# Kernel tuning notes

Measured on AMD Instinct MI355X. Metric: run time of the kernel, lower is better.

Reference implementation:

```python
import jax, jax.numpy as jnp
import numpy as np

EMBED_DIM = 1024
EXPAND_RATIO = 128  # head_dim; n_heads = EMBED_DIM // EXPAND_RATIO = 8
B, N = 4, 2048


def setup_inputs() -> dict:
    key = jax.random.key(0)
    ks = jax.random.split(key, 6)
    std = 0.02
    d = EMBED_DIM
    return {
        "x": jax.random.normal(ks[0], (B, N, d), dtype=jnp.float32),
        "Wq": jax.random.normal(ks[1], (d, d), dtype=jnp.float32) * std,
        "Wk": jax.random.normal(ks[2], (d, d), dtype=jnp.float32) * std,
        "Wv": jax.random.normal(ks[3], (d, d), dtype=jnp.float32) * std,
        "Wo": jax.random.normal(ks[4], (d, d), dtype=jnp.float32) * std,
        "norm_w": jnp.ones((d,), dtype=jnp.float32),
    }


def _rmsnorm(x, w, eps=1e-6):
    return x * jax.lax.rsqrt(jnp.mean(x * x, axis=-1, keepdims=True) + eps) * w


def _gla_scan(q, k, v, g):
    # q,k,v,g: [b, n, h, d]; state S: [b, h, d_k, d_v]
    b, n, h, d = q.shape
    qs, ks_, vs, gs = (jnp.moveaxis(t, 1, 0) for t in (q, k, v, g))  # [n,b,h,d]
    S0 = jnp.zeros((b, h, d, d), dtype=q.dtype)

    def step(S, inp):
        q_t, k_t, v_t, g_t = inp
        # S_t = diag(exp(g_t)) S_{t-1} + k_t^T v_t (gate on key dim)
        S = jnp.exp(g_t)[..., :, None] * S + k_t[..., :, None] * v_t[..., None, :]
        o_t = jnp.einsum('bhk,bhkv->bhv', q_t, S)
        return S, o_t

    _, outs = jax.lax.scan(step, S0, (qs, ks_, vs, gs))
    return jnp.moveaxis(outs, 0, 1)  # [b, n, h, d]


def reference(x, Wq, Wk, Wv, Wo, norm_w):
    b, n, D = x.shape
    hd = EXPAND_RATIO
    h = D // hd

    q = jax.nn.silu(x @ Wq.T)          # q_activation = silu
    f = jax.nn.sigmoid(x @ Wk.T)       # f = sigmoid(k_proj(x))
    log_f = jax.nn.log_sigmoid(f)      # faithful: logsigmoid applied to f (lower_bound=None path)
    k = 1.0 - f
    v = x @ Wv.T

    def split_heads(t):
        return t.reshape(b, n, h, hd)

    out = _gla_scan(split_heads(q), split_heads(k), split_heads(v), split_heads(log_f))
    out = out.reshape(b, n, D)
    out = _rmsnorm(out, norm_w)        # norm_pos='ogate', no output gate
    return out @ Wo.T
```

## Files before the change

kernel.cpp:

```cpp
#include <hip/hip_runtime.h>
#include <cstdint>
#include <cstddef>


typedef unsigned short u16;
using f32x4  = __attribute__((ext_vector_type(4))) float;
using bf16x8 = __attribute__((ext_vector_type(8))) short;

__device__ __forceinline__ float bf2f(u16 u) {
  union { unsigned int i; float f; } v; v.i = ((unsigned int)u) << 16; return v.f;
}
__device__ __forceinline__ u16 f2bf(float f) {
  union { float f; unsigned int i; } v; v.f = f;
  unsigned int r = v.i + 0x7fffu + ((v.i >> 16) & 1u);
  return (u16)(r >> 16);
}
__device__ __forceinline__ void async_load16(const void* g, void* l) {
  __builtin_amdgcn_global_load_lds(
      (const __attribute__((address_space(1))) unsigned int*)(uintptr_t)g,
      (__attribute__((address_space(3))) unsigned int*)(uintptr_t)l, 16, 0, 0);
}
__device__ __forceinline__ float logsig01(float f) {
  float u = f * f;
  return -0.69314718f + 0.5f * f + u * (-0.125f + u * (0.0052083335f - u * 3.472222e-4f));
}

__device__ __forceinline__ void gemm128_core(const u16* __restrict__ Ag, const u16* __restrict__ Bg,
                                             u16* smem, f32x4 (&acc)[4][4]) {
  const int tid = threadIdx.x;
  const int lane = tid & 63, wave = tid >> 6;
  const int wm = (wave & 1) * 64, wn = (wave >> 1) * 64;
  const int r = lane & 15, quad = lane >> 4;
  const int xk = (r >> 1) & 3;
  const u16* baseA = smem + (wm + r) * 32 + ((quad ^ xk) & 3) * 8;
  const u16* baseB = smem + 4096 + (wn + r) * 32 + ((quad ^ xk) & 3) * 8;
  const int soff = (tid >> 2) * 1024 + (((tid & 3) ^ ((tid >> 3) & 3)) * 8);
  u16* dA = smem + wave * 512;
  u16* dB = smem + 4096 + wave * 512;
#pragma unroll
  for (int it = 0; it < 2; ++it) {
    async_load16(Ag + it * 65536 + soff, dA + it * 2048);
    async_load16(Bg + it * 65536 + soff, dB + it * 2048);
  }
#pragma unroll 2
  for (int kt = 0; kt < 32; ++kt) {
    const int cb = (kt & 1) * 8192;
    __syncthreads();
    if (kt < 31) {
      const int nb = ((kt + 1) & 1) * 8192;
      const u16* As = Ag + (kt + 1) * 32 + soff;
      const u16* Bs = Bg + (kt + 1) * 32 + soff;
#pragma unroll
      for (int it = 0; it < 2; ++it) {
        async_load16(As + it * 65536, dA + nb + it * 2048);
        async_load16(Bs + it * 65536, dB + nb + it * 2048);
      }
    }
    bf16x8 af[4], bv[4];
#pragma unroll
    for (int i = 0; i < 4; ++i) af[i] = *(const bf16x8*)(baseA + cb + i * 512);
#pragma unroll
    for (int j = 0; j < 4; ++j) bv[j] = *(const bf16x8*)(baseB + cb + j * 512);
#pragma unroll
    for (int i = 0; i < 4; ++i)
#pragma unroll
      for (int j = 0; j < 4; ++j)
        acc[i][j] = __builtin_amdgcn_mfma_f32_16x16x32_bf16(af[i], bv[j], acc[i][j], 0, 0, 0);
  }
}

__device__ __forceinline__ void gemm64_core(const u16* __restrict__ Ag, const u16* __restrict__ Bg,
                                            u16* smem, f32x4 (&acc)[2][4]) {
  const int tid = threadIdx.x;
  const int lane = tid & 63, wave = tid >> 6;
  const int wm = (wave & 1) * 32, wn = (wave >> 1) * 64;
  const int r = lane & 15, quad = lane >> 4;
  const int xk = (r >> 1) & 3;
  const u16* baseA = smem + (wm + r) * 32 + ((quad ^ xk) & 3) * 8;
  const u16* baseB = smem + 2048 + (wn + r) * 32 + ((quad ^ xk) & 3) * 8;
  const int soff = (tid >> 2) * 1024 + (((tid & 3) ^ ((tid >> 3) & 3)) * 8);
  u16* dA = smem + wave * 512;
  u16* dB = smem + 2048 + wave * 512;
  async_load16(Ag + soff, dA);
  async_load16(Bg + soff, dB);
  async_load16(Bg + 65536 + soff, dB + 2048);
#pragma unroll 2
  for (int kt = 0; kt < 32; ++kt) {
    const int cb = (kt & 1) * 6144;
    __syncthreads();
    if (kt < 31) {
      const int nb = ((kt + 1) & 1) * 6144;
      const u16* As = Ag + (kt + 1) * 32 + soff;
      const u16* Bs = Bg + (kt + 1) * 32 + soff;
      async_load16(As, dA + nb);
      async_load16(Bs, dB + nb);
      async_load16(Bs + 65536, dB + nb + 2048);
    }
    bf16x8 af[2], bv[4];
#pragma unroll
    for (int i = 0; i < 2; ++i) af[i] = *(const bf16x8*)(baseA + cb + i * 512);
#pragma unroll
    for (int j = 0; j < 4; ++j) bv[j] = *(const bf16x8*)(baseB + cb + j * 512);
#pragma unroll
    for (int i = 0; i < 2; ++i)
#pragma unroll
      for (int j = 0; j < 4; ++j)
        acc[i][j] = __builtin_amdgcn_mfma_f32_16x16x32_bf16(af[i], bv[j], acc[i][j], 0, 0, 0);
  }
}

__global__ __launch_bounds__(256) void cast_all(
    const float* __restrict__ x, const float* __restrict__ w0, const float* __restrict__ w1,
    const float* __restrict__ w2, const float* __restrict__ w3, const float* __restrict__ nw,
    u16* __restrict__ xd, u16* __restrict__ d0, u16* __restrict__ d1,
    u16* __restrict__ d2, u16* __restrict__ d3, float* __restrict__ Sv) {
  const int blk = blockIdx.x;
  if (blk >= 12288) {
    Sv[(blk - 12288) * 256 + threadIdx.x] = 0.f;
    return;
  }
  const float* src;
  u16* dst;
  int i;
  bool fold = false;
  if (blk < 8192) {
    src = x; dst = xd; i = blk * 256 + threadIdx.x;
  } else {
    int wb = blk - 8192, which = wb >> 10;
    i = (wb & 1023) * 256 + threadIdx.x;
    src = which == 0 ? w0 : (which == 1 ? w1 : (which == 2 ? w2 : w3));
    dst = which == 0 ? d0 : (which == 1 ? d1 : (which == 2 ? d2 : d3));
    fold = (which == 3);
  }
  float4 v = ((const float4*)src)[i];
  if (fold) {
    float4 wv = ((const float4*)nw)[i & 255];
    v.x *= wv.x; v.y *= wv.y; v.z *= wv.z; v.w *= wv.w;
  }
  unsigned int lo = (unsigned)f2bf(v.x) | ((unsigned)f2bf(v.y) << 16);
  unsigned int hi = (unsigned)f2bf(v.z) | ((unsigned)f2bf(v.w) << 16);
  ((uint2*)dst)[i] = make_uint2(lo, hi);
}

__global__ __launch_bounds__(256) void hgru_gemm_qkv(
    const u16* __restrict__ Xb, const u16* __restrict__ Wqb, const u16* __restrict__ Wkb,
    const u16* __restrict__ Wvb, u16* __restrict__ Qb, u16* __restrict__ Kb,
    u16* __restrict__ Vb) {
  __shared__ alignas(16) u16 smem[12288];
  const int which = blockIdx.y >> 3, bn = blockIdx.y & 7;
  const u16* W = which == 0 ? Wqb : (which == 1 ? Wkb : Wvb);
  const u16* Ag = Xb + (size_t)blockIdx.x * 64 * 1024;
  const u16* Bg = W + (size_t)bn * 128 * 1024;
  f32x4 acc[2][4] = {};
  gemm64_core(Ag, Bg, smem, acc);
  const int tid = threadIdx.x, lane = tid & 63, wave = tid >> 6;
  const int wm = (wave & 1) * 32, wn = (wave >> 1) * 64;
  const int r = lane & 15, quad = lane >> 4;

  __syncthreads();
#pragma unroll
  for (int i = 0; i < 2; ++i)
#pragma unroll
    for (int j = 0; j < 4; ++j)
#pragma unroll
      for (int reg = 0; reg < 4; ++reg) {
        int ml = wm + i * 16 + quad * 4 + reg;
        int nl = wn + j * 16 + r;
        float z = acc[i][j][reg];
        float v;
        if (which == 0)      v = z / (1.f + __expf(-z));
        else if (which == 1) { float ek = __expf(-z); v = ek / (1.f + ek); }
        else                 v = z;
        smem[ml * 136 + nl] = f2bf(v);
      }
  __syncthreads();

  u16* __restrict__ dst = which == 0 ? Qb : (which == 1 ? Kb : Vb);
  const int row16 = tid >> 4, seg = tid & 15;
#pragma unroll
  for (int p = 0; p < 4; ++p) {
    int row = row16 + p * 16;
    *(uint4*)(dst + (size_t)(blockIdx.x * 64 + row) * 1024 + bn * 128 + seg * 8) =
        *(const uint4*)(smem + row * 136 + seg * 8);
  }
}

__global__ __launch_bounds__(256, 4) void hgru_scan(
    const u16* __restrict__ Qg, const u16* __restrict__ Kg, const u16* __restrict__ Vg,
    u16* __restrict__ O, float* __restrict__ Ssum) {
  __shared__ alignas(16) char smem[40448];
  u16* sKt  = (u16*)(smem);
  u16* sVt1 = (u16*)(smem + 10240);
  u16* sK   = (u16*)(smem + 15360);
  u16* sQ   = (u16*)(smem + 24064);
  u16* sVt2 = (u16*)(smem + 32768);
  u16* sAm  = (u16*)(smem + 37888);
  u16* sU   = (u16*)(smem);
  u16* sO   = (u16*)(smem + 17408);

  const int tid = threadIdx.x, blk = blockIdx.x;
  const int vh = blk & 1, c = (blk >> 1) & 63, bh = blk >> 7, h = bh & 7, bb_ = bh >> 3;
  const size_t rb = (size_t)(bb_ * 2048 + c * 32) * 1024 + h * 128;
  const bool haveP = (c > 0);
  const size_t rb1 = haveP ? rb - 32 * 1024 : rb;

  const int lane = tid & 63, wave = tid >> 6;
  const int r = lane & 15, quad = lane >> 4;
  const int ts = tid & 31, g8 = tid >> 5;

  uint4 V2 = *(const uint4*)(Vg + rb  + (size_t)ts * 1024 + vh * 64 + g8 * 8);
  uint4 V1 = *(const uint4*)(Vg + rb1 + (size_t)ts * 1024 + vh * 64 + g8 * 8);
  { const u16* vp = (const u16*)&V2;
#pragma unroll
    for (int e = 0; e < 8; ++e) sVt2[(g8 * 8 + e) * 40 + ts] = vp[e]; }
  if (haveP) {
    const u16* vp = (const u16*)&V1;
#pragma unroll
    for (int e = 0; e < 8; ++e) sVt1[(g8 * 8 + e) * 40 + ts] = vp[e];
  }

  const int col = tid & 127;
  if (tid < 128) {
    if (haveP) {
      const u16* kc = Kg + rb1 + col;
      unsigned int kraw[16];
      float bC = 0.f;
#pragma unroll
      for (int t = 0; t < 16; ++t) {
        unsigned int a = kc[(size_t)(2 * t) * 1024];
        unsigned int b = kc[(size_t)(2 * t + 1) * 1024];
        kraw[t] = a | (b << 16);
        bC += logsig01(1.f - bf2f((u16)a)) + logsig01(1.f - bf2f((u16)b));
      }
      float run = 0.f;
#pragma unroll
      for (int t = 0; t < 16; ++t) {
        float ka = bf2f((u16)(kraw[t] & 0xffff));
        float kb = bf2f((u16)(kraw[t] >> 16));
        run += logsig01(1.f - ka);
        sKt[col * 40 + 2 * t]     = f2bf(ka * __expf(bC - run));
        run += logsig01(1.f - kb);
        sKt[col * 40 + 2 * t + 1] = f2bf(kb * __expf(bC - run));
      }
    }
  } else {
    const u16* kc = Kg + rb + col;
    const u16* qc = Qg + rb + col;
    float run = 0.f;
#pragma unroll
    for (int t = 0; t < 32; ++t) {
      u16 ku = kc[(size_t)t * 1024];
      u16 qu = qc[(size_t)t * 1024];
      float kv = bf2f(ku);
      run += logsig01(1.f - kv);
      sQ[t * 136 + col] = f2bf(bf2f(qu) * __expf(run));
      sK[t * 136 + col] = f2bf(kv * __expf(-run));
    }
  }
  __syncthreads();

  f32x4 accU[2][4] = {};
  const int vm = (wave & 1) * 32, in = (wave >> 1) * 64;
  if (haveP) {
#pragma unroll
    for (int mi = 0; mi < 2; ++mi) {
      bf16x8 af = *(const bf16x8*)(sVt1 + (vm + mi * 16 + r) * 40 + quad * 8);
#pragma unroll
      for (int nj = 0; nj < 4; ++nj) {
        bf16x8 bv = *(const bf16x8*)(sKt + (in + nj * 16 + r) * 40 + quad * 8);
        accU[mi][nj] = __builtin_amdgcn_mfma_f32_16x16x32_bf16(af, bv, accU[mi][nj], 0, 0, 0);
      }
    }
  }
  { const int mi = wave & 1, nj = wave >> 1;
    f32x4 a1 = {0.f, 0.f, 0.f, 0.f};
#pragma unroll
    for (int ks = 0; ks < 4; ++ks) {
      bf16x8 af = *(const bf16x8*)(sQ + (mi * 16 + r) * 136 + ks * 32 + quad * 8);
      bf16x8 bk = *(const bf16x8*)(sK + (nj * 16 + r) * 136 + ks * 32 + quad * 8);
      a1 = __builtin_amdgcn_mfma_f32_16x16x32_bf16(af, bk, a1, 0, 0, 0);
    }
#pragma unroll
    for (int reg = 0; reg < 4; ++reg) {
      int t = mi * 16 + quad * 4 + reg, s = nj * 16 + r;
      sAm[t * 40 + s] = (s <= t) ? f2bf(a1[reg]) : (u16)0;
    } }
  __syncthreads();

  if (haveP) {
#pragma unroll
    for (int mi = 0; mi < 2; ++mi)
#pragma unroll
      for (int nj = 0; nj < 4; ++nj)
#pragma unroll
        for (int reg = 0; reg < 4; ++reg) {
          int vl = vm + mi * 16 + quad * 4 + reg;
          int i  = in + nj * 16 + r;
          sU[vl * 136 + i] = f2bf(accU[mi][nj][reg]);
        }
  }
  __syncthreads();

  { const int mi = wave & 1, no = (wave >> 1) * 32;
    bf16x8 af0 = *(const bf16x8*)(sAm + (mi * 16 + r) * 40 + quad * 8);
    bf16x8 afq[4];
    if (haveP) {
#pragma unroll
      for (int ks = 0; ks < 4; ++ks)
        afq[ks] = *(const bf16x8*)(sQ + (mi * 16 + r) * 136 + ks * 32 + quad * 8);
    }
    f32x4 ssq = {0.f, 0.f, 0.f, 0.f};
#pragma unroll
    for (int j = 0; j < 2; ++j) {
      f32x4 acc2 = {0.f, 0.f, 0.f, 0.f};
      bf16x8 bv0 = *(const bf16x8*)(sVt2 + (no + j * 16 + r) * 40 + quad * 8);
      acc2 = __builtin_amdgcn_mfma_f32_16x16x32_bf16(af0, bv0, acc2, 0, 0, 0);
      if (haveP) {
#pragma unroll
        for (int ks = 0; ks < 4; ++ks) {
          bf16x8 bs = *(const bf16x8*)(sU + (no + j * 16 + r) * 136 + ks * 32 + quad * 8);
          acc2 = __builtin_amdgcn_mfma_f32_16x16x32_bf16(afq[ks], bs, acc2, 0, 0, 0);
        }
      }
      ssq += acc2 * acc2;
#pragma unroll
      for (int reg = 0; reg < 4; ++reg) {
        int t = mi * 16 + quad * 4 + reg;
        sO[t * 72 + no + j * 16 + r] = f2bf(acc2[reg]);
      }
    }
    const int rowg = bb_ * 2048 + c * 32 + mi * 16 + quad * 4;
#pragma unroll
    for (int reg = 0; reg < 4; ++reg) {
      float v = ssq[reg];
      v += __shfl_xor(v, 1); v += __shfl_xor(v, 2);
      v += __shfl_xor(v, 4); v += __shfl_xor(v, 8);
      if (r == 0) atomicAdd(&Ssum[rowg + reg], v);
    } }
  __syncthreads();

  { const int row = tid >> 3, seg = tid & 7;
    *(uint4*)(O + rb + (size_t)row * 1024 + vh * 64 + seg * 8) =
        *(const uint4*)(sO + row * 72 + seg * 8); }
}

__global__ __launch_bounds__(256) void hgru_gemm_out(const u16* __restrict__ Ab,
                                                     const u16* __restrict__ Wob,
                                                     const float* __restrict__ Ssum,
                                                     float* __restrict__ out) {
  __shared__ alignas(16) u16 smem[16384];
  const u16* Ag = Ab + (size_t)blockIdx.x * 128 * 1024;
  const u16* Bg = Wob + (size_t)blockIdx.y * 128 * 1024;
  f32x4 acc[4][4] = {};
  gemm128_core(Ag, Bg, smem, acc);
  const int tid = threadIdx.x, lane = tid & 63, wave = tid >> 6;
  const int wm = (wave & 1) * 64, wn = (wave >> 1) * 64;
  const int r = lane & 15, quad = lane >> 4;
#pragma unroll
  for (int i = 0; i < 4; ++i)
#pragma unroll
    for (int reg = 0; reg < 4; ++reg) {
      int m = blockIdx.x * 128 + wm + i * 16 + quad * 4 + reg;
      float sm = rsqrtf(Ssum[m] * (1.f / 1024.f) + 1e-6f);
#pragma unroll
      for (int j = 0; j < 4; ++j) {
        int n = blockIdx.y * 128 + wn + j * 16 + r;
        out[(size_t)m * 1024 + n] = acc[i][j][reg] * sm;
      }
    }
}

extern "C" void kernel_launch(void* const* d_in, const int* in_sizes, int n_in,
                              void* d_out, int out_size, void* d_ws, size_t ws_size,
                              hipStream_t stream) {
  const float* x  = (const float*)d_in[0];
  const float* Wq = (const float*)d_in[1];
  const float* Wk = (const float*)d_in[2];
  const float* Wv = (const float*)d_in[3];
  const float* Wo = (const float*)d_in[4];
  const float* nw = (const float*)d_in[5];
  float* out = (float*)d_out;
  char* ws = (char*)d_ws;

  u16* Xb   = (u16*)(ws + 0);
  u16* Wqb  = (u16*)(ws + 16777216);
  u16* Wkb  = (u16*)(ws + 18874368);
  u16* Wvb  = (u16*)(ws + 20971520);
  u16* Wob  = (u16*)(ws + 23068672);
  u16* Qb   = (u16*)(ws + 25165824);
  u16* Kb   = (u16*)(ws + 41943040);
  u16* Vb   = (u16*)(ws + 58720256);
  u16* Obf  = (u16*)(ws + 75497472);
  float* Sv = (float*)(ws + 92274688);

  cast_all<<<12320, 256, 0, stream>>>(x, Wq, Wk, Wv, Wo, nw, Xb, Wqb, Wkb, Wvb, Wob, Sv);

  dim3 gq(128, 24);
  hgru_gemm_qkv<<<gq, 256, 0, stream>>>(Xb, Wqb, Wkb, Wvb, Qb, Kb, Vb);
  hgru_scan<<<4096, 256, 0, stream>>>(Qb, Kb, Vb, Obf, Sv);
  dim3 go(64, 8);
  hgru_gemm_out<<<go, 256, 0, stream>>>(Obf, Wob, Sv, out);
}
```

Measured before the change: 245.8 us.

## Enlarge QKV GEMM tile to 256x128 with 512-thread blocks

The QKV projection GEMM moves from 64x128 tiles on 256 threads to 256x128 tiles on 512 threads. Each wave now computes a 64x64 sub-tile with 4x4 MFMA accumulators. This raises arithmetic intensity and reuses each weight tile across four times more rows, cutting global/LDS traffic per FLOP. The epilogue is split into two phases so it can reuse the staging buffer. The trade-off is a grid of only 768 blocks for 256 CUs, more registers per thread, and double the LDS.

New measurement: 617.8 us. +151.4%, slower.

```diff
diff --git a/kernel.cpp b/kernel.cpp
--- a/kernel.cpp
+++ b/kernel.cpp
@@ -69,46 +69,6 @@
   }
 }
 
-__device__ __forceinline__ void gemm64_core(const u16* __restrict__ Ag, const u16* __restrict__ Bg,
-                                            u16* smem, f32x4 (&acc)[2][4]) {
-  const int tid = threadIdx.x;
-  const int lane = tid & 63, wave = tid >> 6;
-  const int wm = (wave & 1) * 32, wn = (wave >> 1) * 64;
-  const int r = lane & 15, quad = lane >> 4;
-  const int xk = (r >> 1) & 3;
-  const u16* baseA = smem + (wm + r) * 32 + ((quad ^ xk) & 3) * 8;
-  const u16* baseB = smem + 2048 + (wn + r) * 32 + ((quad ^ xk) & 3) * 8;
-  const int soff = (tid >> 2) * 1024 + (((tid & 3) ^ ((tid >> 3) & 3)) * 8);
-  u16* dA = smem + wave * 512;
-  u16* dB = smem + 2048 + wave * 512;
-  async_load16(Ag + soff, dA);
-  async_load16(Bg + soff, dB);
-  async_load16(Bg + 65536 + soff, dB + 2048);
-#pragma unroll 2
-  for (int kt = 0; kt < 32; ++kt) {
-    const int cb = (kt & 1) * 6144;
-    __syncthreads();
-    if (kt < 31) {
-      const int nb = ((kt + 1) & 1) * 6144;
-      const u16* As = Ag + (kt + 1) * 32 + soff;
-      const u16* Bs = Bg + (kt + 1) * 32 + soff;
-      async_load16(As, dA + nb);
-      async_load16(Bs, dB + nb);
-      async_load16(Bs + 65536, dB + nb + 2048);
-    }
-    bf16x8 af[2], bv[4];
-#pragma unroll
-    for (int i = 0; i < 2; ++i) af[i] = *(const bf16x8*)(baseA + cb + i * 512);
-#pragma unroll
-    for (int j = 0; j < 4; ++j) bv[j] = *(const bf16x8*)(baseB + cb + j * 512);
-#pragma unroll
-    for (int i = 0; i < 2; ++i)
-#pragma unroll
-      for (int j = 0; j < 4; ++j)
-        acc[i][j] = __builtin_amdgcn_mfma_f32_16x16x32_bf16(af[i], bv[j], acc[i][j], 0, 0, 0);
-  }
-}
-
 __global__ __launch_bounds__(256) void cast_all(
     const float* __restrict__ x, const float* __restrict__ w0, const float* __restrict__ w1,
     const float* __restrict__ w2, const float* __restrict__ w3, const float* __restrict__ nw,
@@ -142,46 +102,87 @@
   ((uint2*)dst)[i] = make_uint2(lo, hi);
 }
 
-__global__ __launch_bounds__(256) void hgru_gemm_qkv(
+__global__ __launch_bounds__(512, 6) void hgru_gemm_qkv(
     const u16* __restrict__ Xb, const u16* __restrict__ Wqb, const u16* __restrict__ Wkb,
     const u16* __restrict__ Wvb, u16* __restrict__ Qb, u16* __restrict__ Kb,
     u16* __restrict__ Vb) {
-  __shared__ alignas(16) u16 smem[12288];
+  __shared__ alignas(16) u16 smem[24576];
   const int which = blockIdx.y >> 3, bn = blockIdx.y & 7;
   const u16* W = which == 0 ? Wqb : (which == 1 ? Wkb : Wvb);
-  const u16* Ag = Xb + (size_t)blockIdx.x * 64 * 1024;
+  const u16* Ag = Xb + (size_t)blockIdx.x * 256 * 1024;
   const u16* Bg = W + (size_t)bn * 128 * 1024;
-  f32x4 acc[2][4] = {};
-  gemm64_core(Ag, Bg, smem, acc);
-  const int tid = threadIdx.x, lane = tid & 63, wave = tid >> 6;
-  const int wm = (wave & 1) * 32, wn = (wave >> 1) * 64;
+
+  const int tid = threadIdx.x;
+  const int lane = tid & 63, wave = tid >> 6;
+  const int wr = wave >> 1, wc = wave & 1;
   const int r = lane & 15, quad = lane >> 4;
-
-  __syncthreads();
-#pragma unroll
-  for (int i = 0; i < 2; ++i)
-#pragma unroll
-    for (int j = 0; j < 4; ++j)
-#pragma unroll
-      for (int reg = 0; reg < 4; ++reg) {
-        int ml = wm + i * 16 + quad * 4 + reg;
-        int nl = wn + j * 16 + r;
-        float z = acc[i][j][reg];
-        float v;
-        if (which == 0)      v = z / (1.f + __expf(-z));
-        else if (which == 1) { float ek = __expf(-z); v = ek / (1.f + ek); }
-        else                 v = z;
-        smem[ml * 136 + nl] = f2bf(v);
-      }
-  __syncthreads();
+  const int xk = (r >> 1) & 3;
+  const u16* baseA = smem + (wr * 64 + r) * 32 + ((quad ^ xk) & 3) * 8;
+  const u16* baseB = smem + 8192 + (wc * 64 + r) * 32 + ((quad ^ xk) & 3) * 8;
+  const int soff = (tid >> 2) * 1024 + (((tid & 3) ^ ((tid >> 3) & 3)) * 8);
+  u16* dA = smem + wave * 512;
+  u16* dB = smem + 8192 + wave * 512;
+
+  f32x4 acc[4][4] = {};
+
+  async_load16(Ag + soff, dA);
+  async_load16(Ag + 131072 + soff, dA + 4096);
+  async_load16(Bg + soff, dB);
+
+#pragma unroll 2
+  for (int kt = 0; kt < 32; ++kt) {
+    const int cb = (kt & 1) * 12288;
+    __syncthreads();
+    if (kt < 31) {
+      const int nb = ((kt + 1) & 1) * 12288;
+      const u16* As = Ag + (kt + 1) * 32 + soff;
+      async_load16(As, dA + nb);
+      async_load16(As + 131072, dA + nb + 4096);
+      async_load16(Bg + (kt + 1) * 32 + soff, dB + nb);
+    }
+    bf16x8 af[4], bv[4];
+#pragma unroll
+    for (int i = 0; i < 4; ++i) af[i] = *(const bf16x8*)(baseA + cb + i * 512);
+#pragma unroll
+    for (int j = 0; j < 4; ++j) bv[j] = *(const bf16x8*)(baseB + cb + j * 512);
+#pragma unroll
+    for (int i = 0; i < 4; ++i)
+#pragma unroll
+      for (int j = 0; j < 4; ++j)
+        acc[i][j] = __builtin_amdgcn_mfma_f32_16x16x32_bf16(af[i], bv[j], acc[i][j], 0, 0, 0);
+  }
 
   u16* __restrict__ dst = which == 0 ? Qb : (which == 1 ? Kb : Vb);
-  const int row16 = tid >> 4, seg = tid & 15;
-#pragma unroll
-  for (int p = 0; p < 4; ++p) {
-    int row = row16 + p * 16;
-    *(uint4*)(dst + (size_t)(blockIdx.x * 64 + row) * 1024 + bn * 128 + seg * 8) =
-        *(const uint4*)(smem + row * 136 + seg * 8);
+  const int row32 = tid >> 4, seg = tid & 15;
+#pragma unroll
+  for (int ph = 0; ph < 2; ++ph) {
+    __syncthreads();
+    if ((wr >> 1) == ph) {
+      const int mbase = (wr & 1) * 64;
+#pragma unroll
+      for (int i = 0; i < 4; ++i)
+#pragma unroll
+        for (int j = 0; j < 4; ++j)
+#pragma unroll
+          for (int reg = 0; reg < 4; ++reg) {
+            int ml = mbase + i * 16 + quad * 4 + reg;
+            int nl = wc * 64 + j * 16 + r;
+            float z = acc[i][j][reg];
+            float v;
+            if (which == 0)      v = z / (1.f + __expf(-z));
+            else if (which == 1) { float ek = __expf(-z); v = ek / (1.f + ek); }
+            else                 v = z;
+            smem[ml * 136 + nl] = f2bf(v);
+          }
+    }
+    __syncthreads();
+#pragma unroll
+    for (int p = 0; p < 4; ++p) {
+      int row = row32 + p * 32;
+      int grow = blockIdx.x * 256 + ph * 128 + row;
+      *(uint4*)(dst + (size_t)grow * 1024 + bn * 128 + seg * 8) =
+          *(const uint4*)(smem + row * 136 + seg * 8);
+    }
   }
 }
 
@@ -395,8 +396,8 @@
 
   cast_all<<<12320, 256, 0, stream>>>(x, Wq, Wk, Wv, Wo, nw, Xb, Wqb, Wkb, Wvb, Wob, Sv);
 
-  dim3 gq(128, 24);
-  hgru_gemm_qkv<<<gq, 256, 0, stream>>>(Xb, Wqb, Wkb, Wvb, Qb, Kb, Vb);
+  dim3 gq(32, 24);
+  hgru_gemm_qkv<<<gq, 512, 0, stream>>>(Xb, Wqb, Wkb, Wvb, Qb, Kb, Vb);
   hgru_scan<<<4096, 256, 0, stream>>>(Qb, Kb, Vb, Obf, Sv);
   dim3 go(64, 8);
   hgru_gemm_out<<<go, 256, 0, stream>>>(Obf, Wob, Sv, out);
```
